# Optimization experiments

Hardware: AMD Instinct MI355X
Metric: run time of the kernel (lower is better)

The kernel has to match this reference:

```python
import jax, jax.numpy as jnp
import numpy as np

DIM = 1024
HEADS = 16
HEAD_DIM = DIM // HEADS


def setup_inputs() -> dict:
    key = jax.random.key(0)
    ks = jax.random.split(key, 5)
    x = jax.random.normal(ks[0], (4, 2048, DIM), dtype=jnp.float32)
    # nn.Linear params: weight [out, in], bias [out]
    w_qkv = jax.random.normal(ks[1], (3 * DIM, DIM), dtype=jnp.float32) * (DIM ** -0.5)
    b_qkv = jnp.zeros((3 * DIM,), dtype=jnp.float32)
    w_proj = jax.random.normal(ks[2], (DIM, DIM), dtype=jnp.float32) * (DIM ** -0.5)
    b_proj = jnp.zeros((DIM,), dtype=jnp.float32)
    return {"x": x, "w_qkv": w_qkv, "b_qkv": b_qkv, "w_proj": w_proj, "b_proj": b_proj}


def reference(x, w_qkv, b_qkv, w_proj, b_proj):
    B, S, D = x.shape
    scale = HEAD_DIM ** -0.5
    qkv = x @ w_qkv.T + b_qkv                       # [B,S,3D]
    qkv = qkv.reshape(B, S, 3, HEADS, HEAD_DIM)
    qkv = jnp.transpose(qkv, (2, 0, 3, 1, 4))       # [3,B,H,S,hd]
    q, k, v = qkv[0], qkv[1], qkv[2]
    attn = jnp.einsum("bhqd,bhkd->bhqk", q, k) * scale
    attn = jax.nn.softmax(attn, axis=-1)
    out = jnp.einsum("bhqk,bhkd->bhqd", attn, v)    # [B,H,S,hd]
    out = jnp.transpose(out, (0, 2, 1, 3)).reshape(B, S, D)
    return out @ w_proj.T + b_proj
```

## Files before the change

kernel.cpp:

```cpp
#include <hip/hip_runtime.h>
#include <hip/hip_bf16.h>
#include <stdint.h>

#define SEQ 2048
#define NBH 64
#define HD 64

typedef __bf16     bx8   __attribute__((ext_vector_type(8)));
typedef float      fx4   __attribute__((ext_vector_type(4)));
typedef float      f32x16 __attribute__((ext_vector_type(16)));
typedef uint32_t   ux2   __attribute__((ext_vector_type(2)));
typedef unsigned short us8 __attribute__((ext_vector_type(8)));

__device__ __forceinline__ float bf2f(unsigned short u){
  uint32_t x = ((uint32_t)u) << 16; return __builtin_bit_cast(float, x);
}
__device__ __forceinline__ unsigned short f2bf_rne(float f){
  uint32_t u = __builtin_bit_cast(uint32_t, f);
  return (unsigned short)((u + 0x7FFFu + ((u >> 16) & 1u)) >> 16);
}
__device__ __forceinline__ uint32_t cvtpk(float lo, float hi){
  uint32_t r; asm("v_cvt_pk_bf16_f32 %0, %1, %2" : "=v"(r) : "v"(lo), "v"(hi));
  return r;
}

typedef __attribute__((address_space(3))) void  lvoid;
typedef const __attribute__((address_space(1))) void gvoid;
__device__ __forceinline__ void gll16(const void* g, void* l){
  __builtin_amdgcn_global_load_lds((gvoid*)(uintptr_t)g,
                                   (lvoid*)(uint32_t)(uintptr_t)l, 16, 0, 0);
}

template<int OFF>
__device__ __forceinline__ ux2 tr16(uint32_t addr){
  ux2 d;
  asm volatile("ds_read_b64_tr_b16 %0, %1 offset:%2" : "=v"(d) : "v"(addr), "i"(OFF));
  return d;
}
__device__ __forceinline__ bx8 mk8(ux2 a, ux2 b){
  union { uint32_t u[4]; bx8 v; } U;
  U.u[0]=a[0]; U.u[1]=a[1]; U.u[2]=b[0]; U.u[3]=b[1];
  return U.v;
}
__device__ __forceinline__ bx8 mk8u(uint32_t u0, uint32_t u1, uint32_t u2, uint32_t u3){
  union { uint32_t u[4]; bx8 v; } U;
  U.u[0]=u0; U.u[1]=u1; U.u[2]=u2; U.u[3]=u3;
  return U.v;
}

__global__ void castk(const float* __restrict__ in, unsigned short* __restrict__ out, int n){
  int i = (blockIdx.x * 256 + threadIdx.x) * 8;
  if (i + 7 < n){
    const float4* p = (const float4*)(in + i);
    float4 a = p[0], b = p[1];
    us8 r;
    r[0]=f2bf_rne(a.x); r[1]=f2bf_rne(a.y); r[2]=f2bf_rne(a.z); r[3]=f2bf_rne(a.w);
    r[4]=f2bf_rne(b.x); r[5]=f2bf_rne(b.y); r[6]=f2bf_rne(b.z); r[7]=f2bf_rne(b.w);
    *(us8*)(out + i) = r;
  }
}

template<int EPI>
__global__ __launch_bounds__(256, 2) void gemm_bt(
    const unsigned short* __restrict__ A, const unsigned short* __restrict__ Bw,
    const float* __restrict__ bias, void* __restrict__ outp,
    int M, int N, int K)
{
  __shared__ __align__(16) unsigned short Al[2][128*64];
  __shared__ __align__(16) unsigned short Bl[2][128*64];
  const int tid = threadIdx.x;
  const int w = tid >> 6, l = tid & 63;
  const int l15 = l & 15, lg = l >> 4;
  const int wr = w >> 1, wc = w & 1;
  const int brow = blockIdx.y * 128, bcol = blockIdx.x * 128;

  fx4 acc[4][4];
  #pragma unroll
  for (int m = 0; m < 4; m++)
    #pragma unroll
    for (int n = 0; n < 4; n++) acc[m][n] = (fx4){0.f,0.f,0.f,0.f};

  auto stage = [&](int buf, int k0){
    #pragma unroll
    for (int i = 0; i < 4; i++){
      int g = i*256 + tid; int row = g >> 3; int c = (g & 7) ^ (row & 7);
      gll16(A + (size_t)(brow + row) * K + k0 + c*8, &Al[buf][g*8]);
    }
    #pragma unroll
    for (int i = 0; i < 4; i++){
      int g = i*256 + tid; int row = g >> 3; int c = (g & 7) ^ (row & 7);
      gll16(Bw + (size_t)(bcol + row) * K + k0 + c*8, &Bl[buf][g*8]);
    }
  };

  stage(0, 0);
  int cur = 0;
  for (int k0 = 0; k0 < K; k0 += 64){
    if (k0 + 64 < K){
      stage(cur ^ 1, k0 + 64);
      asm volatile("s_waitcnt vmcnt(8)" ::: "memory");
    } else {
      asm volatile("s_waitcnt vmcnt(0)" ::: "memory");
    }
    __builtin_amdgcn_s_barrier();

    bx8 af[4][2], bf[4][2];
    #pragma unroll
    for (int kc = 0; kc < 2; kc++){
      #pragma unroll
      for (int m = 0; m < 4; m++){
        int row = wr*64 + m*16 + l15;
        int ch  = (kc*4 + lg) ^ (row & 7);
        af[m][kc] = *(const bx8*)&Al[cur][row*64 + ch*8];
      }
      #pragma unroll
      for (int n = 0; n < 4; n++){
        int row = wc*64 + n*16 + l15;
        int ch  = (kc*4 + lg) ^ (row & 7);
        bf[n][kc] = *(const bx8*)&Bl[cur][row*64 + ch*8];
      }
    }
    #pragma unroll
    for (int kc = 0; kc < 2; kc++)
      #pragma unroll
      for (int m = 0; m < 4; m++)
        #pragma unroll
        for (int n = 0; n < 4; n++)
          acc[m][n] = __builtin_amdgcn_mfma_f32_16x16x32_bf16(af[m][kc], bf[n][kc], acc[m][n], 0, 0, 0);
    __builtin_amdgcn_s_barrier();
    cur ^= 1;
  }

  #pragma unroll
  for (int m = 0; m < 4; m++){
    int row0 = brow + wr*64 + m*16 + lg*4;
    #pragma unroll
    for (int n = 0; n < 4; n++){
      int col = bcol + wc*64 + n*16 + l15;
      float bq = bias[col];
      if (EPI == 0){
        int which = col >> 10, rem = col & 1023, h = rem >> 6, d = rem & 63;
        #pragma unroll
        for (int i = 0; i < 4; i++){
          int r = row0 + i; int b = r >> 11, s = r & 2047;
          size_t idx = (((size_t)which*64 + (size_t)b*16 + h) * 2048 + s) * 64 + d;
          ((unsigned short*)outp)[idx] = f2bf_rne(acc[m][n][i] + bq);
        }
      } else {
        #pragma unroll
        for (int i = 0; i < 4; i++){
          int r = row0 + i;
          ((float*)outp)[(size_t)r * N + col] = acc[m][n][i] + bq;
        }
      }
    }
  }
}

__global__ __launch_bounds__(256, 4) void attn_k(const unsigned short* __restrict__ qkv,
                                                 unsigned short* __restrict__ ob)
{
  __shared__ __align__(16) unsigned short Kl[2][64*64];
  __shared__ __align__(16) unsigned short Vl[2][64*64];
  __shared__ float lsc[4][32];
  const int tid = threadIdx.x, w = tid >> 6, l = tid & 63;
  const int l31 = l & 31, hi = l >> 5, l15 = l & 15;
  const int flat = blockIdx.y * 16 + blockIdx.x;
  const int nid  = (flat & 7) * 128 + (flat >> 3);
  const int qblk = nid & 15, bh = nid >> 4;
  const unsigned short* Qh = qkv + (size_t)bh * SEQ * HD;
  const unsigned short* Kh = qkv + (size_t)(NBH + bh) * SEQ * HD;
  const unsigned short* Vh = qkv + (size_t)(2*NBH + bh) * SEQ * HD;
  const int q0 = qblk * 128;

  const int g0 = tid, g1 = 256 + tid;
  const int kr0 = g0 >> 3, kc0 = ((g0 & 7) ^ (kr0 & 7));
  const int kr1 = g1 >> 3, kc1 = ((g1 & 7) ^ (kr1 & 7));
  const int kb0 = kr0*64 + kc0*8, kb1 = kr1*64 + kc1*8;
  const int e0 = g0*8, e1 = g1*8;
  const int vb0 = ((e0 >> 4) & 63)*64 + (e0 >> 10)*16 + (e0 & 15);
  const int vb1 = ((e1 >> 4) & 63)*64 + (e1 >> 10)*16 + (e1 & 15);

  unsigned short* KlF = &Kl[0][0];
  #pragma unroll
  for (int i = 0; i < 4; i++){
    int g = i*256 + tid; int row = g >> 3; int c = (g & 7) ^ (row & 7);
    gll16(Qh + (size_t)(q0 + row) * 64 + c*8, &KlF[g*8]);
  }
  asm volatile("s_waitcnt vmcnt(0)" ::: "memory");
  __syncthreads();
  bx8 qf[4];
  {
    int qrow = w*32 + l31;
    #pragma unroll
    for (int dk = 0; dk < 4; dk++){
      int ch = (dk*2 + hi) ^ (qrow & 7);
      qf[dk] = *(const bx8*)&KlF[qrow*64 + ch*8];
    }
  }
  __syncthreads();

  auto stage = [&](int buf, int t){
    const unsigned short* kp = Kh + t*4096;
    const unsigned short* vp = Vh + t*4096;
    gll16(kp + kb0, &Kl[buf][g0*8]);
    gll16(kp + kb1, &Kl[buf][g1*8]);
    gll16(vp + vb0, &Vl[buf][e0]);
    gll16(vp + vb1, &Vl[buf][e1]);
  };

  const float SCL = 0.125f * 1.44269504f;
  const float MB  = 24.0f;
  float lsum = 0.f;
  f32x16 acco[2] = {};

  stage(0, 0);
  int cur = 0;
  const uint32_t vlane = (uint32_t)((l31 >> 4)*2048 + hi*256 + l15*8);

  for (int t = 0; t < SEQ/64; t++){
    if (t + 1 < SEQ/64){
      stage(cur ^ 1, t + 1);
      asm volatile("s_waitcnt vmcnt(4)" ::: "memory");
    } else {
      asm volatile("s_waitcnt vmcnt(0)" ::: "memory");
    }
    __builtin_amdgcn_s_barrier();

    const uint32_t vbb = (uint32_t)(uintptr_t)&Vl[cur][0];
    bx8 pa[4];

    f32x16 sb0 = {}, sb1 = {};
    __builtin_amdgcn_s_setprio(1);
    #pragma unroll
    for (int dk = 0; dk < 4; dk++){
      int ch = (dk*2 + hi) ^ (l31 & 7);
      bx8 a0 = *(const bx8*)&Kl[cur][l31*64 + ch*8];
      sb0 = __builtin_amdgcn_mfma_f32_32x32x16_bf16(a0, qf[dk], sb0, 0, 0, 0);
    }
    #pragma unroll
    for (int dk = 0; dk < 4; dk++){
      int ch = (dk*2 + hi) ^ (l31 & 7);
      bx8 a1 = *(const bx8*)&Kl[cur][(32 + l31)*64 + ch*8];
      sb1 = __builtin_amdgcn_mfma_f32_32x32x16_bf16(a1, qf[dk], sb1, 0, 0, 0);
    }
    __builtin_amdgcn_s_setprio(0);

    #pragma unroll
    for (int r = 0; r < 16; r++){
      float p = __builtin_amdgcn_exp2f(__builtin_fmaf(sb0[r], SCL, -MB));
      sb0[r] = p; lsum += p;
    }
    #pragma unroll
    for (int hf = 0; hf < 2; hf++){
      const int r0 = hf * 8;
      uint32_t c01 = cvtpk(sb0[r0+0], sb0[r0+1]);
      uint32_t c23 = cvtpk(sb0[r0+2], sb0[r0+3]);
      uint32_t c45 = cvtpk(sb0[r0+4], sb0[r0+5]);
      uint32_t c67 = cvtpk(sb0[r0+6], sb0[r0+7]);
      asm("v_permlane32_swap_b32 %0, %1" : "+v"(c01), "+v"(c45));
      asm("v_permlane32_swap_b32 %0, %1" : "+v"(c23), "+v"(c67));
      pa[hf] = mk8u(c01, c23, c45, c67);
    }

    ux2 vrA[2][2][2];
    #pragma unroll
    for (int kvs = 0; kvs < 2; kvs++)
      #pragma unroll
      for (int db = 0; db < 2; db++){
        uint32_t a = vbb + vlane + db*4096 + kvs*512;
        vrA[kvs][db][0] = tr16<0>(a);
        vrA[kvs][db][1] = tr16<128>(a);
      }

    #pragma unroll
    for (int r = 0; r < 16; r++){
      float p = __builtin_amdgcn_exp2f(__builtin_fmaf(sb1[r], SCL, -MB));
      sb1[r] = p; lsum += p;
    }
    #pragma unroll
    for (int hf = 0; hf < 2; hf++){
      const int r0 = hf * 8;
      uint32_t c01 = cvtpk(sb1[r0+0], sb1[r0+1]);
      uint32_t c23 = cvtpk(sb1[r0+2], sb1[r0+3]);
      uint32_t c45 = cvtpk(sb1[r0+4], sb1[r0+5]);
      uint32_t c67 = cvtpk(sb1[r0+6], sb1[r0+7]);
      asm("v_permlane32_swap_b32 %0, %1" : "+v"(c01), "+v"(c45));
      asm("v_permlane32_swap_b32 %0, %1" : "+v"(c23), "+v"(c67));
      pa[2 + hf] = mk8u(c01, c23, c45, c67);
    }

    ux2 vrB[2][2][2];
    #pragma unroll
    for (int kvs = 0; kvs < 2; kvs++)
      #pragma unroll
      for (int db = 0; db < 2; db++){
        uint32_t a = vbb + vlane + db*4096 + (kvs + 2)*512;
        vrB[kvs][db][0] = tr16<0>(a);
        vrB[kvs][db][1] = tr16<128>(a);
      }

    asm volatile("s_waitcnt lgkmcnt(8)" ::: "memory");
    __builtin_amdgcn_sched_barrier(0);
    __builtin_amdgcn_s_setprio(1);
    #pragma unroll
    for (int kvs = 0; kvs < 2; kvs++)
      #pragma unroll
      for (int db = 0; db < 2; db++)
        acco[db] = __builtin_amdgcn_mfma_f32_32x32x16_bf16(
            pa[kvs], mk8(vrA[kvs][db][0], vrA[kvs][db][1]), acco[db], 0, 0, 0);
    __builtin_amdgcn_s_setprio(0);
    asm volatile("s_waitcnt lgkmcnt(0)" ::: "memory");
    __builtin_amdgcn_sched_barrier(0);
    __builtin_amdgcn_s_setprio(1);
    #pragma unroll
    for (int kvs = 0; kvs < 2; kvs++)
      #pragma unroll
      for (int db = 0; db < 2; db++)
        acco[db] = __builtin_amdgcn_mfma_f32_32x32x16_bf16(
            pa[2 + kvs], mk8(vrB[kvs][db][0], vrB[kvs][db][1]), acco[db], 0, 0, 0);
    __builtin_amdgcn_s_setprio(0);
    __builtin_amdgcn_s_barrier();
    cur ^= 1;
  }

  float lsf = lsum + __shfl_xor(lsum, 32);
  lsc[w][l31] = lsf;
  float inv[16];
  #pragma unroll
  for (int r = 0; r < 16; r++){
    int q = (r & 3) + 8*(r >> 2) + 4*hi;
    inv[r] = 1.0f / lsc[w][q];
  }
  const int b = bh >> 4, h = bh & 15;
  #pragma unroll
  for (int r = 0; r < 16; r++){
    int qg = q0 + w*32 + (r & 3) + 8*(r >> 2) + 4*hi;
    size_t base = ((size_t)b * 2048 + qg) * 1024 + h*64;
    ob[base + l31]      = f2bf_rne(acco[0][r] * inv[r]);
    ob[base + 32 + l31] = f2bf_rne(acco[1][r] * inv[r]);
  }
}

extern "C" void kernel_launch(void* const* d_in, const int* in_sizes, int n_in,
                              void* d_out, int out_size, void* d_ws, size_t ws_size,
                              hipStream_t stream) {
  const float* x     = (const float*)d_in[0];
  const float* wqkv  = (const float*)d_in[1];
  const float* bqkv  = (const float*)d_in[2];
  const float* wproj = (const float*)d_in[3];
  const float* bproj = (const float*)d_in[4];
  float* out = (float*)d_out;

  char* ws = (char*)d_ws;
  unsigned short* xb     = (unsigned short*)(ws);
  unsigned short* obuf   = (unsigned short*)(ws + 16777216);
  unsigned short* wqkvb  = (unsigned short*)(ws + 33554432);
  unsigned short* wprojb = (unsigned short*)(ws + 39845888);
  unsigned short* qkvb   = (unsigned short*)(ws + 41943040);

  castk<<<dim3(4096), dim3(256), 0, stream>>>(x,     xb,     8388608);
  castk<<<dim3(1536), dim3(256), 0, stream>>>(wqkv,  wqkvb,  3145728);
  castk<<<dim3(512),  dim3(256), 0, stream>>>(wproj, wprojb, 1048576);

  gemm_bt<0><<<dim3(24, 64), dim3(256), 0, stream>>>(xb, wqkvb, bqkv, (void*)qkvb, 8192, 3072, 1024);
  attn_k    <<<dim3(16, 64), dim3(256), 0, stream>>>(qkvb, obuf);
  gemm_bt<1><<<dim3(8, 64),  dim3(256), 0, stream>>>(obuf, wprojb, bproj, (void*)out, 8192, 1024, 1024);
}
```

Baseline: 186.4 us.

## Use 256x256-tile 512-thread QKV GEMM with interleaved staging and XCD-aware block remap

Replaces the templated 128x128 GEMM for the QKV projection with a dedicated 256x256-tile, 8-wave kernel. Next-tile global-to-LDS loads are split into halves and interleaved between the MFMA groups, s_setprio raises priority around the MFMAs, and block IDs are remapped across the 8 XCDs. The larger tile raises data reuse per LDS load and cuts global traffic. In exchange it uses 128 KB of LDS and more accumulator registers, which can lower occupancy, and gives only 384 blocks.

Result: no change. 190.1 us (+2.0%).

```diff
diff --git a/kernel.cpp b/kernel.cpp
--- a/kernel.cpp
+++ b/kernel.cpp
@@ -60,10 +60,161 @@
   }
 }
 
-template<int EPI>
-__global__ __launch_bounds__(256, 2) void gemm_bt(
+__global__ __launch_bounds__(512, 2) void gemm256_qkv(
     const unsigned short* __restrict__ A, const unsigned short* __restrict__ Bw,
-    const float* __restrict__ bias, void* __restrict__ outp,
+    const float* __restrict__ bias, unsigned short* __restrict__ outp, int K)
+{
+  __shared__ __align__(16) unsigned short Al[2][256*64];
+  __shared__ __align__(16) unsigned short Bl[2][256*64];
+  const int tid = threadIdx.x;
+  const int w = tid >> 6, l = tid & 63;
+  const int l15 = l & 15, lg = l >> 4;
+  const int wr = w >> 2, wc = w & 3;
+  const int flat = blockIdx.y * gridDim.x + blockIdx.x;
+  const int cpx = (gridDim.x * gridDim.y) >> 3;
+  const int nid = (flat & 7) * cpx + (flat >> 3);
+  const int bx = nid % gridDim.x, by = nid / gridDim.x;
+  const int brow = by * 256, bcol = bx * 256;
+
+  fx4 acc[8][4];
+  #pragma unroll
+  for (int m = 0; m < 8; m++)
+    #pragma unroll
+    for (int n = 0; n < 4; n++) acc[m][n] = (fx4){0.f,0.f,0.f,0.f};
+
+  auto stageA = [&](int buf, int k0, int half){
+    #pragma unroll
+    for (int i = 0; i < 2; i++){
+      int g = (half*2 + i)*512 + tid;
+      int row = g >> 3, c = (g & 7) ^ (row & 7);
+      gll16(A + (size_t)(brow + row) * K + k0 + c*8, &Al[buf][g*8]);
+    }
+  };
+  auto stageB = [&](int buf, int k0, int half){
+    #pragma unroll
+    for (int i = 0; i < 2; i++){
+      int g = (half*2 + i)*512 + tid;
+      int row = g >> 3, c = (g & 7) ^ (row & 7);
+      gll16(Bw + (size_t)(bcol + row) * K + k0 + c*8, &Bl[buf][g*8]);
+    }
+  };
+
+  stageA(0, 0, 0); stageA(0, 0, 1);
+  stageB(0, 0, 0); stageB(0, 0, 1);
+
+  int cur = 0;
+  for (int k0 = 0; k0 < K; k0 += 64){
+    const bool pre = (k0 + 64 < K);
+    const int nk = k0 + 64;
+    if (pre){
+      stageA(cur ^ 1, nk, 0);
+      asm volatile("s_waitcnt vmcnt(2)" ::: "memory");
+    } else {
+      asm volatile("s_waitcnt vmcnt(0)" ::: "memory");
+    }
+    __builtin_amdgcn_s_barrier();
+    __builtin_amdgcn_sched_barrier(0);
+
+    bx8 bfr[2][4];
+    #pragma unroll
+    for (int n = 0; n < 4; n++){
+      int row = wc*64 + n*16 + l15;
+      bfr[0][n] = *(const bx8*)&Bl[cur][row*64 + (lg ^ (row & 7))*8];
+    }
+    {
+      bx8 af[4];
+      #pragma unroll
+      for (int m = 0; m < 4; m++){
+        int row = wr*128 + m*16 + l15;
+        af[m] = *(const bx8*)&Al[cur][row*64 + (lg ^ (row & 7))*8];
+      }
+      __builtin_amdgcn_s_setprio(1);
+      #pragma unroll
+      for (int m = 0; m < 4; m++)
+        #pragma unroll
+        for (int n = 0; n < 4; n++)
+          acc[m][n] = __builtin_amdgcn_mfma_f32_16x16x32_bf16(af[m], bfr[0][n], acc[m][n], 0, 0, 0);
+      __builtin_amdgcn_s_setprio(0);
+    }
+    if (pre) stageA(cur ^ 1, nk, 1);
+    #pragma unroll
+    for (int n = 0; n < 4; n++){
+      int row = wc*64 + n*16 + l15;
+      bfr[1][n] = *(const bx8*)&Bl[cur][row*64 + ((4 + lg) ^ (row & 7))*8];
+    }
+    {
+      bx8 af[4];
+      #pragma unroll
+      for (int m = 0; m < 4; m++){
+        int row = wr*128 + m*16 + l15;
+        af[m] = *(const bx8*)&Al[cur][row*64 + ((4 + lg) ^ (row & 7))*8];
+      }
+      __builtin_amdgcn_s_setprio(1);
+      #pragma unroll
+      for (int m = 0; m < 4; m++)
+        #pragma unroll
+        for (int n = 0; n < 4; n++)
+          acc[m][n] = __builtin_amdgcn_mfma_f32_16x16x32_bf16(af[m], bfr[1][n], acc[m][n], 0, 0, 0);
+      __builtin_amdgcn_s_setprio(0);
+    }
+    if (pre) stageB(cur ^ 1, nk, 0);
+    {
+      bx8 af[4];
+      #pragma unroll
+      for (int m = 0; m < 4; m++){
+        int row = wr*128 + (m + 4)*16 + l15;
+        af[m] = *(const bx8*)&Al[cur][row*64 + (lg ^ (row & 7))*8];
+      }
+      __builtin_amdgcn_s_setprio(1);
+      #pragma unroll
+      for (int m = 0; m < 4; m++)
+        #pragma unroll
+        for (int n = 0; n < 4; n++)
+          acc[m + 4][n] = __builtin_amdgcn_mfma_f32_16x16x32_bf16(af[m], bfr[0][n], acc[m + 4][n], 0, 0, 0);
+      __builtin_amdgcn_s_setprio(0);
+    }
+    if (pre) stageB(cur ^ 1, nk, 1);
+    {
+      bx8 af[4];
+      #pragma unroll
+      for (int m = 0; m < 4; m++){
+        int row = wr*128 + (m + 4)*16 + l15;
+        af[m] = *(const bx8*)&Al[cur][row*64 + ((4 + lg) ^ (row & 7))*8];
+      }
+      __builtin_amdgcn_s_setprio(1);
+      #pragma unroll
+      for (int m = 0; m < 4; m++)
+        #pragma unroll
+        for (int n = 0; n < 4; n++)
+          acc[m + 4][n] = __builtin_amdgcn_mfma_f32_16x16x32_bf16(af[m], bfr[1][n], acc[m + 4][n], 0, 0, 0);
+      __builtin_amdgcn_s_setprio(0);
+    }
+    asm volatile("" ::: "memory");
+    __builtin_amdgcn_s_barrier();
+    cur ^= 1;
+  }
+
+  #pragma unroll
+  for (int m = 0; m < 8; m++){
+    int row0 = brow + wr*128 + m*16 + lg*4;
+    #pragma unroll
+    for (int n = 0; n < 4; n++){
+      int col = bcol + wc*64 + n*16 + l15;
+      float bq = bias[col];
+      int which = col >> 10, rem = col & 1023, h = rem >> 6, d = rem & 63;
+      #pragma unroll
+      for (int i = 0; i < 4; i++){
+        int r = row0 + i; int b = r >> 11, s = r & 2047;
+        size_t idx = (((size_t)which*64 + (size_t)b*16 + h) * 2048 + s) * 64 + d;
+        outp[idx] = f2bf_rne(acc[m][n][i] + bq);
+      }
+    }
+  }
+}
+
+__global__ __launch_bounds__(256, 2) void gemm_proj(
+    const unsigned short* __restrict__ A, const unsigned short* __restrict__ Bw,
+    const float* __restrict__ bias, float* __restrict__ outp,
     int M, int N, int K)
 {
   __shared__ __align__(16) unsigned short Al[2][128*64];
@@ -138,20 +289,10 @@
     for (int n = 0; n < 4; n++){
       int col = bcol + wc*64 + n*16 + l15;
       float bq = bias[col];
-      if (EPI == 0){
-        int which = col >> 10, rem = col & 1023, h = rem >> 6, d = rem & 63;
-        #pragma unroll
-        for (int i = 0; i < 4; i++){
-          int r = row0 + i; int b = r >> 11, s = r & 2047;
-          size_t idx = (((size_t)which*64 + (size_t)b*16 + h) * 2048 + s) * 64 + d;
-          ((unsigned short*)outp)[idx] = f2bf_rne(acc[m][n][i] + bq);
-        }
-      } else {
-        #pragma unroll
-        for (int i = 0; i < 4; i++){
-          int r = row0 + i;
-          ((float*)outp)[(size_t)r * N + col] = acc[m][n][i] + bq;
-        }
+      #pragma unroll
+      for (int i = 0; i < 4; i++){
+        int r = row0 + i;
+        outp[(size_t)r * N + col] = acc[m][n][i] + bq;
       }
     }
   }
@@ -363,7 +504,7 @@
   castk<<<dim3(1536), dim3(256), 0, stream>>>(wqkv,  wqkvb,  3145728);
   castk<<<dim3(512),  dim3(256), 0, stream>>>(wproj, wprojb, 1048576);
 
-  gemm_bt<0><<<dim3(24, 64), dim3(256), 0, stream>>>(xb, wqkvb, bqkv, (void*)qkvb, 8192, 3072, 1024);
-  attn_k    <<<dim3(16, 64), dim3(256), 0, stream>>>(qkvb, obuf);
-  gemm_bt<1><<<dim3(8, 64),  dim3(256), 0, stream>>>(obuf, wprojb, bproj, (void*)out, 8192, 1024, 1024);
-}
+  gemm256_qkv<<<dim3(12, 32), dim3(512), 0, stream>>>(xb, wqkvb, bqkv, qkvb, 1024);
+  attn_k     <<<dim3(16, 64), dim3(256), 0, stream>>>(qkvb, obuf);
+  gemm_proj  <<<dim3(8, 64),  dim3(256), 0, stream>>>(obuf, wprojb, bproj, out, 8192, 1024, 1024);
+}
```

## Use 256x128 GEMM tiles with 8 waves, interleaved prefetch and XCD-aware block remap

Applied to the files above, without the earlier changes.

Both linear-layer GEMMs move to 512-thread blocks computing 256x128 output tiles, which halves the grid rows. Each k-step is split into four phases, and global-to-LDS prefetch of the next tile is interleaved between MFMA bursts that run under raised s_setprio. Block indices are remapped so consecutive blocks land on the same XCD, aiming for better L2 reuse. This adds more barriers per k-step and doubles the A-tile LDS footprint, which could limit occupancy.

Result: slower. 194.4 us (+4.3%).

```diff
diff --git a/kernel.cpp b/kernel.cpp
--- a/kernel.cpp
+++ b/kernel.cpp
@@ -61,18 +61,21 @@
 }
 
 template<int EPI>
-__global__ __launch_bounds__(256, 2) void gemm_bt(
+__global__ __launch_bounds__(512, 2) void gemm256(
     const unsigned short* __restrict__ A, const unsigned short* __restrict__ Bw,
-    const float* __restrict__ bias, void* __restrict__ outp,
-    int M, int N, int K)
+    const float* __restrict__ bias, void* __restrict__ outp, int N, int K)
 {
-  __shared__ __align__(16) unsigned short Al[2][128*64];
+  __shared__ __align__(16) unsigned short Al[2][256*64];
   __shared__ __align__(16) unsigned short Bl[2][128*64];
   const int tid = threadIdx.x;
   const int w = tid >> 6, l = tid & 63;
   const int l15 = l & 15, lg = l >> 4;
   const int wr = w >> 1, wc = w & 1;
-  const int brow = blockIdx.y * 128, bcol = blockIdx.x * 128;
+  const int flat = blockIdx.y * gridDim.x + blockIdx.x;
+  const int cpx = (gridDim.x * gridDim.y) >> 3;
+  const int nid = (flat & 7) * cpx + (flat >> 3);
+  const int bx = nid % gridDim.x, by = nid / gridDim.x;
+  const int brow = by * 256, bcol = bx * 128;
 
   fx4 acc[4][4];
   #pragma unroll
@@ -80,53 +83,105 @@
     #pragma unroll
     for (int n = 0; n < 4; n++) acc[m][n] = (fx4){0.f,0.f,0.f,0.f};
 
-  auto stage = [&](int buf, int k0){
-    #pragma unroll
-    for (int i = 0; i < 4; i++){
-      int g = i*256 + tid; int row = g >> 3; int c = (g & 7) ^ (row & 7);
+  auto stageA = [&](int buf, int k0, int part){
+    #pragma unroll
+    for (int i = 0; i < 2; i++){
+      int g = (part*2 + i)*512 + tid;
+      int row = g >> 3, c = (g & 7) ^ (row & 7);
       gll16(A + (size_t)(brow + row) * K + k0 + c*8, &Al[buf][g*8]);
     }
-    #pragma unroll
-    for (int i = 0; i < 4; i++){
-      int g = i*256 + tid; int row = g >> 3; int c = (g & 7) ^ (row & 7);
+  };
+  auto stageB = [&](int buf, int k0){
+    #pragma unroll
+    for (int i = 0; i < 2; i++){
+      int g = i*512 + tid;
+      int row = g >> 3, c = (g & 7) ^ (row & 7);
       gll16(Bw + (size_t)(bcol + row) * K + k0 + c*8, &Bl[buf][g*8]);
     }
   };
 
-  stage(0, 0);
+  stageA(0, 0, 0); stageA(0, 0, 1); stageB(0, 0);
+  asm volatile("s_waitcnt vmcnt(0)" ::: "memory");
+  __builtin_amdgcn_s_barrier();
+
   int cur = 0;
   for (int k0 = 0; k0 < K; k0 += 64){
-    if (k0 + 64 < K){
-      stage(cur ^ 1, k0 + 64);
-      asm volatile("s_waitcnt vmcnt(8)" ::: "memory");
-    } else {
-      asm volatile("s_waitcnt vmcnt(0)" ::: "memory");
-    }
-    __builtin_amdgcn_s_barrier();
-
-    bx8 af[4][2], bf[4][2];
-    #pragma unroll
-    for (int kc = 0; kc < 2; kc++){
-      #pragma unroll
-      for (int m = 0; m < 4; m++){
-        int row = wr*64 + m*16 + l15;
-        int ch  = (kc*4 + lg) ^ (row & 7);
-        af[m][kc] = *(const bx8*)&Al[cur][row*64 + ch*8];
-      }
-      #pragma unroll
-      for (int n = 0; n < 4; n++){
-        int row = wc*64 + n*16 + l15;
-        int ch  = (kc*4 + lg) ^ (row & 7);
-        bf[n][kc] = *(const bx8*)&Bl[cur][row*64 + ch*8];
-      }
-    }
-    #pragma unroll
-    for (int kc = 0; kc < 2; kc++)
-      #pragma unroll
-      for (int m = 0; m < 4; m++)
-        #pragma unroll
-        for (int n = 0; n < 4; n++)
-          acc[m][n] = __builtin_amdgcn_mfma_f32_16x16x32_bf16(af[m][kc], bf[n][kc], acc[m][n], 0, 0, 0);
+    const bool pre = (k0 + 64 < K);
+    const int nk = k0 + 64;
+    bx8 bfr[4], afr[2];
+
+    #pragma unroll
+    for (int n = 0; n < 4; n++){
+      int row = wc*64 + n*16 + l15;
+      bfr[n] = *(const bx8*)&Bl[cur][row*64 + (lg ^ (row & 7))*8];
+    }
+    #pragma unroll
+    for (int m = 0; m < 2; m++){
+      int row = wr*64 + m*16 + l15;
+      afr[m] = *(const bx8*)&Al[cur][row*64 + (lg ^ (row & 7))*8];
+    }
+    if (pre) stageA(cur ^ 1, nk, 0);
+    __builtin_amdgcn_s_barrier();
+    __builtin_amdgcn_s_setprio(1);
+    #pragma unroll
+    for (int m = 0; m < 2; m++)
+      #pragma unroll
+      for (int n = 0; n < 4; n++)
+        acc[m][n] = __builtin_amdgcn_mfma_f32_16x16x32_bf16(afr[m], bfr[n], acc[m][n], 0, 0, 0);
+    __builtin_amdgcn_s_setprio(0);
+    __builtin_amdgcn_s_barrier();
+
+    #pragma unroll
+    for (int m = 0; m < 2; m++){
+      int row = wr*64 + (m + 2)*16 + l15;
+      afr[m] = *(const bx8*)&Al[cur][row*64 + (lg ^ (row & 7))*8];
+    }
+    if (pre) stageA(cur ^ 1, nk, 1);
+    __builtin_amdgcn_s_barrier();
+    __builtin_amdgcn_s_setprio(1);
+    #pragma unroll
+    for (int m = 0; m < 2; m++)
+      #pragma unroll
+      for (int n = 0; n < 4; n++)
+        acc[m + 2][n] = __builtin_amdgcn_mfma_f32_16x16x32_bf16(afr[m], bfr[n], acc[m + 2][n], 0, 0, 0);
+    __builtin_amdgcn_s_setprio(0);
+    __builtin_amdgcn_s_barrier();
+
+    #pragma unroll
+    for (int n = 0; n < 4; n++){
+      int row = wc*64 + n*16 + l15;
+      bfr[n] = *(const bx8*)&Bl[cur][row*64 + ((4 + lg) ^ (row & 7))*8];
+    }
+    #pragma unroll
+    for (int m = 0; m < 2; m++){
+      int row = wr*64 + m*16 + l15;
+      afr[m] = *(const bx8*)&Al[cur][row*64 + ((4 + lg) ^ (row & 7))*8];
+    }
+    if (pre) stageB(cur ^ 1, nk);
+    __builtin_amdgcn_s_barrier();
+    __builtin_amdgcn_s_setprio(1);
+    #pragma unroll
+    for (int m = 0; m < 2; m++)
+      #pragma unroll
+      for (int n = 0; n < 4; n++)
+        acc[m][n] = __builtin_amdgcn_mfma_f32_16x16x32_bf16(afr[m], bfr[n], acc[m][n], 0, 0, 0);
+    __builtin_amdgcn_s_setprio(0);
+    __builtin_amdgcn_s_barrier();
+
+    #pragma unroll
+    for (int m = 0; m < 2; m++){
+      int row = wr*64 + (m + 2)*16 + l15;
+      afr[m] = *(const bx8*)&Al[cur][row*64 + ((4 + lg) ^ (row & 7))*8];
+    }
+    __builtin_amdgcn_s_barrier();
+    __builtin_amdgcn_s_setprio(1);
+    #pragma unroll
+    for (int m = 0; m < 2; m++)
+      #pragma unroll
+      for (int n = 0; n < 4; n++)
+        acc[m + 2][n] = __builtin_amdgcn_mfma_f32_16x16x32_bf16(afr[m], bfr[n], acc[m + 2][n], 0, 0, 0);
+    __builtin_amdgcn_s_setprio(0);
+    asm volatile("s_waitcnt vmcnt(0)" ::: "memory");
     __builtin_amdgcn_s_barrier();
     cur ^= 1;
   }
@@ -363,7 +418,7 @@
   castk<<<dim3(1536), dim3(256), 0, stream>>>(wqkv,  wqkvb,  3145728);
   castk<<<dim3(512),  dim3(256), 0, stream>>>(wproj, wprojb, 1048576);
 
-  gemm_bt<0><<<dim3(24, 64), dim3(256), 0, stream>>>(xb, wqkvb, bqkv, (void*)qkvb, 8192, 3072, 1024);
+  gemm256<0><<<dim3(24, 32), dim3(512), 0, stream>>>(xb, wqkvb, bqkv, (void*)qkvb, 3072, 1024);
   attn_k    <<<dim3(16, 64), dim3(256), 0, stream>>>(qkvb, obuf);
-  gemm_bt<1><<<dim3(8, 64),  dim3(256), 0, stream>>>(obuf, wprojb, bproj, (void*)out, 8192, 1024, 1024);
-}
+  gemm256<1><<<dim3(8, 32),  dim3(512), 0, stream>>>(obuf, wprojb, bproj, (void*)out, 1024, 1024);
+}
```

## Double attention workgroup to 512 threads, 256 query rows per block

Applied to the files above, without the earlier changes.

The attention kernel now runs 8 waves per workgroup, each handling 32 query rows, so one block covers 256 queries and every staged K/V tile is shared by twice as many waves. Each thread now issues one global-to-LDS load per tile instead of two, halving total K/V traffic per query. Q fragments are loaded straight from global memory into registers, replacing the LDS staging round trip. Occupancy drops to 2 blocks of 512 threads per CU, and the grid shrinks to 512 blocks, which can leave CUs underfilled.

After: 180.3 us. -3.3%, faster.

```diff
diff --git a/kernel.cpp b/kernel.cpp
--- a/kernel.cpp
+++ b/kernel.cpp
@@ -157,56 +157,41 @@
   }
 }
 
-__global__ __launch_bounds__(256, 4) void attn_k(const unsigned short* __restrict__ qkv,
+__global__ __launch_bounds__(512, 2) void attn_k(const unsigned short* __restrict__ qkv,
                                                  unsigned short* __restrict__ ob)
 {
   __shared__ __align__(16) unsigned short Kl[2][64*64];
   __shared__ __align__(16) unsigned short Vl[2][64*64];
-  __shared__ float lsc[4][32];
+  __shared__ float lsc[8][32];
   const int tid = threadIdx.x, w = tid >> 6, l = tid & 63;
   const int l31 = l & 31, hi = l >> 5, l15 = l & 15;
-  const int flat = blockIdx.y * 16 + blockIdx.x;
-  const int nid  = (flat & 7) * 128 + (flat >> 3);
-  const int qblk = nid & 15, bh = nid >> 4;
+  const int flat = blockIdx.y * 8 + blockIdx.x;
+  const int nid  = (flat & 7) * 64 + (flat >> 3);
+  const int qblk = nid & 7, bh = nid >> 3;
   const unsigned short* Qh = qkv + (size_t)bh * SEQ * HD;
   const unsigned short* Kh = qkv + (size_t)(NBH + bh) * SEQ * HD;
   const unsigned short* Vh = qkv + (size_t)(2*NBH + bh) * SEQ * HD;
-  const int q0 = qblk * 128;
-
-  const int g0 = tid, g1 = 256 + tid;
-  const int kr0 = g0 >> 3, kc0 = ((g0 & 7) ^ (kr0 & 7));
-  const int kr1 = g1 >> 3, kc1 = ((g1 & 7) ^ (kr1 & 7));
-  const int kb0 = kr0*64 + kc0*8, kb1 = kr1*64 + kc1*8;
-  const int e0 = g0*8, e1 = g1*8;
+  const int q0 = qblk * 256;
+
+  const int kr0 = tid >> 3, kc0 = ((tid & 7) ^ (kr0 & 7));
+  const int kb0 = kr0*64 + kc0*8;
+  const int e0 = tid*8;
   const int vb0 = ((e0 >> 4) & 63)*64 + (e0 >> 10)*16 + (e0 & 15);
-  const int vb1 = ((e1 >> 4) & 63)*64 + (e1 >> 10)*16 + (e1 & 15);
-
-  unsigned short* KlF = &Kl[0][0];
-  #pragma unroll
-  for (int i = 0; i < 4; i++){
-    int g = i*256 + tid; int row = g >> 3; int c = (g & 7) ^ (row & 7);
-    gll16(Qh + (size_t)(q0 + row) * 64 + c*8, &KlF[g*8]);
-  }
-  asm volatile("s_waitcnt vmcnt(0)" ::: "memory");
-  __syncthreads();
+
   bx8 qf[4];
   {
-    int qrow = w*32 + l31;
-    #pragma unroll
-    for (int dk = 0; dk < 4; dk++){
-      int ch = (dk*2 + hi) ^ (qrow & 7);
-      qf[dk] = *(const bx8*)&KlF[qrow*64 + ch*8];
-    }
-  }
-  __syncthreads();
+    int qrow = q0 + w*32 + l31;
+    const unsigned short* qp = Qh + (size_t)qrow * 64 + hi*8;
+    #pragma unroll
+    for (int dk = 0; dk < 4; dk++)
+      qf[dk] = *(const bx8*)(qp + dk*16);
+  }
 
   auto stage = [&](int buf, int t){
     const unsigned short* kp = Kh + t*4096;
     const unsigned short* vp = Vh + t*4096;
-    gll16(kp + kb0, &Kl[buf][g0*8]);
-    gll16(kp + kb1, &Kl[buf][g1*8]);
+    gll16(kp + kb0, &Kl[buf][tid*8]);
     gll16(vp + vb0, &Vl[buf][e0]);
-    gll16(vp + vb1, &Vl[buf][e1]);
   };
 
   const float SCL = 0.125f * 1.44269504f;
@@ -221,7 +206,7 @@
   for (int t = 0; t < SEQ/64; t++){
     if (t + 1 < SEQ/64){
       stage(cur ^ 1, t + 1);
-      asm volatile("s_waitcnt vmcnt(4)" ::: "memory");
+      asm volatile("s_waitcnt vmcnt(2)" ::: "memory");
     } else {
       asm volatile("s_waitcnt vmcnt(0)" ::: "memory");
     }
@@ -364,6 +349,6 @@
   castk<<<dim3(512),  dim3(256), 0, stream>>>(wproj, wprojb, 1048576);
 
   gemm_bt<0><<<dim3(24, 64), dim3(256), 0, stream>>>(xb, wqkvb, bqkv, (void*)qkvb, 8192, 3072, 1024);
-  attn_k    <<<dim3(16, 64), dim3(256), 0, stream>>>(qkvb, obuf);
+  attn_k    <<<dim3(8, 64),  dim3(512), 0, stream>>>(qkvb, obuf);
   gemm_bt<1><<<dim3(8, 64),  dim3(256), 0, stream>>>(obuf, wprojb, bproj, (void*)out, 8192, 1024, 1024);
 }
```
